# Performance work log

Hardware: AMD Instinct MI355X
Metric: run time of the kernel (lower is better)

## Reference

```python
import jax, jax.numpy as jnp
import numpy as np

CLASSES, SIZE, INPUT_SIZE, CONTEXT_SIZE, BATCH = 8, 512, 512, 512, 64
CMS = 4          # context_map_size -> 2**CMS = 16 contexts per neuron
LR = 0.01
PRED_CLIP = 0.01
WEIGHT_CLIP = 5.0


def _logit(x):
    return jnp.log(x) - jnp.log1p(-x)


def setup_inputs() -> dict:
    key = jax.random.key(0)
    k1, k2, k3, k4, k5 = jax.random.split(key, 5)
    logits = jax.random.normal(k1, (CLASSES, INPUT_SIZE, BATCH), jnp.float32)
    context = jax.random.normal(k2, (BATCH, CONTEXT_SIZE), jnp.float32)
    target = jax.random.uniform(k3, (CLASSES, BATCH), jnp.float32)
    cmaps = jax.random.normal(k4, (CLASSES, SIZE, CMS, CONTEXT_SIZE), jnp.float32)
    cmaps = cmaps / jnp.linalg.norm(cmaps, axis=-1, keepdims=True)
    cbias = jax.random.normal(k5, (CLASSES, SIZE, CMS, 1), jnp.float32)
    weights = jnp.full((CLASSES, SIZE, 2 ** CMS, INPUT_SIZE), 1.0 / INPUT_SIZE, jnp.float32)
    return {"logits": logits, "context": context, "target": target,
            "context_maps": cmaps, "context_bias": cbias, "weights": weights}


def reference(logits, context, target, context_maps, context_bias, weights):
    # --- context hashing ---
    # distances: [classes, size, cms, batch]
    distances = jnp.einsum('cskd,bd->cskb', context_maps, context)
    bits = (distances > context_bias).astype(jnp.int32)
    conv = (2 ** jnp.arange(CMS, dtype=jnp.int32))[:, None]          # [cms, 1]
    idx = jnp.sum(bits * conv, axis=-2)                              # [classes, size, batch]
    # --- gather per-context weights ---
    c = jnp.arange(CLASSES)[:, None, None]
    s = jnp.arange(SIZE)[None, :, None]
    sel = weights[c, s, idx, :]                                      # [classes, size, batch, input]
    # --- per-sample dot product (== diagonal of the original batch x batch matmul) ---
    lo = _logit(jnp.float32(PRED_CLIP))
    hi = _logit(jnp.float32(1.0 - PRED_CLIP))
    out = jnp.clip(jnp.einsum('csbi,cib->csb', sel, logits), lo, hi)  # [classes, size, batch]
    # --- online weight update (clamped) scattered back ---
    sig = jax.nn.sigmoid(out)
    diff = sig - target[:, None, :]                                  # [classes, size, batch]
    # lr * diff[c,s,b] * logits[c,i,b]  -> update [c,s,b,i]
    upd = LR * diff[:, :, :, None] * jnp.transpose(logits, (0, 2, 1))[:, None, :, :]
    new_sel = jnp.clip(sel - upd, -WEIGHT_CLIP, WEIGHT_CLIP)
    new_weights = weights.at[c, s, idx, :].set(new_sel)
    return out, new_weights
```

## Files before the change

kernel.cpp:

```cpp
#include <hip/hip_runtime.h>
#include <math.h>

#define CLASSES 8
#define SIZE 512
#define ISZ 512
#define CSZ 512
#define BATCH 64
#define CMS 4
#define NBUCKET 16
#define LR 0.01f
#define WCLIP 5.0f
#define WSTRIDE 516

typedef float nt_f4 __attribute__((ext_vector_type(4)));

__global__ __launch_bounds__(256) void pack_pre(
    const float* __restrict__ logits,
    const float* __restrict__ context,
    float* __restrict__ Lt,
    float* __restrict__ Lpk,
    float* __restrict__ ctxT4)
{
    __shared__ float t[64][65];
    const int bid  = blockIdx.x;
    const int lane = threadIdx.x & 63;
    const int w    = threadIdx.x >> 6;
    if (bid < 64) {
        const int r0 = bid << 6;
        #pragma unroll
        for (int rep = 0; rep < 16; ++rep) {
            int rr = w * 16 + rep;
            t[rr][lane] = logits[(size_t)(r0 + rr) * 64 + lane];
        }
        __syncthreads();
        const int ci = r0 + lane;
        #pragma unroll
        for (int rep = 0; rep < 16; ++rep) {
            int b = w * 16 + rep;
            float v = t[lane][b];
            Lt[(size_t)b * 4096 + ci] = v;
            Lpk[(size_t)(ci >> 2) * 256 + 4 * b + (ci & 3)] = v;
        }
    } else {
        const int c0 = (bid - 64) << 6;
        #pragma unroll
        for (int rep = 0; rep < 16; ++rep) {
            int rr = w * 16 + rep;
            t[rr][lane] = context[(size_t)rr * 512 + c0 + lane];
        }
        __syncthreads();
        #pragma unroll
        for (int rep = 0; rep < 16; ++rep) {
            int dd = c0 + w * 16 + rep;
            ctxT4[(size_t)(dd >> 2) * 256 + 4 * lane + (dd & 3)] = t[lane][w * 16 + rep];
        }
    }
}

__global__ __launch_bounds__(256, 8) void dist_kernel(
    const float* __restrict__ cmaps,
    const float* __restrict__ cbias,
    const float* __restrict__ ctxT4,
    unsigned char* __restrict__ idxOut)
{
    __shared__ int bits[CMS * BATCH];

    const int tid  = threadIdx.x;
    const int cs   = blockIdx.x;
    const int lane = tid & 63;
    const int wv   = tid >> 6;
    const int k    = __builtin_amdgcn_readfirstlane(wv);

    const float4* cmg = (const float4*)(cmaps + ((size_t)cs * CMS + k) * CSZ);
    {
        const float4* ct4 = (const float4*)ctxT4 + lane;
        float acc = 0.f;
        #pragma unroll 4
        for (int d4 = 0; d4 < 128; ++d4) {
            float4 cm4 = cmg[d4];
            float4 cv  = ct4[(size_t)d4 * 64];
            acc += cm4.x * cv.x + cm4.y * cv.y + cm4.z * cv.z + cm4.w * cv.w;
        }
        float bias = cbias[(size_t)cs * CMS + k];
        bits[k * BATCH + lane] = (acc > bias) ? 1 : 0;
    }
    __syncthreads();

    if (wv == 0) {
        int idx_b = bits[lane] | (bits[BATCH + lane] << 1) |
                    (bits[2 * BATCH + lane] << 2) | (bits[3 * BATCH + lane] << 3);
        idxOut[(size_t)cs * BATCH + lane] = (unsigned char)idx_b;
    }
}

__global__ __launch_bounds__(256, 4) void gln_bc(
    const float* __restrict__ target,
    const float* __restrict__ weights,
    const unsigned char* __restrict__ idxIn,
    const float* __restrict__ Lt,
    const float* __restrict__ Lpk,
    float* __restrict__ out,
    float* __restrict__ outW)
{
    __shared__ float Wl[NBUCKET * WSTRIDE];
    __shared__ float partial[4 * BATCH];
    __shared__ float diff_l[BATCH];

    const int tid  = threadIdx.x;
    const int cs   = blockIdx.x;
    const int c    = cs >> 9;
    const int lane = tid & 63;
    const int wv   = tid >> 6;

    float4 wreg[8];
    const float4* gW = (const float4*)(weights + (size_t)cs * (NBUCKET * ISZ));
    #pragma unroll
    for (int it = 0; it < 8; ++it) wreg[it] = gW[tid + it * 256];

    const int idx_b = idxIn[(size_t)cs * BATCH + lane];

    int blast_r[16];
    #pragma unroll
    for (int j = 0; j < NBUCKET; ++j) {
        unsigned long long m = __ballot(idx_b == j);
        blast_r[j] = m ? (63 - __clzll(m)) : -1;
    }

    const float* LtC = Lt + (size_t)c * ISZ;
    const int col4 = tid & 127;
    const int hi_half = (tid >> 7) & 1;
    float4 lreg[8];
    int    blv[8];
    #pragma unroll
    for (int it = 0; it < 8; ++it) {
        int bl = hi_half ? blast_r[2 * it + 1] : blast_r[2 * it];
        blv[it] = bl;
        int blc = (bl >= 0) ? bl : 0;
        lreg[it] = ((const float4*)(LtC + (size_t)blc * 4096))[col4];
    }

    #pragma unroll
    for (int it = 0; it < 8; ++it) {
        int f = tid + it * 256;
        *(float4*)&Wl[(f >> 7) * WSTRIDE + (f & 127) * 4] = wreg[it];
    }
    __syncthreads();

    {
        const float4* Lp4 = (const float4*)Lpk;
        const int base4 = (c * 128 + wv * 32) * 64 + lane;
        const int wb    = idx_b * WSTRIDE + wv * 128;
        float acc = 0.f;
        #pragma unroll 4
        for (int d4 = 0; d4 < 32; ++d4) {
            float4 w4 = *(const float4*)&Wl[wb + d4 * 4];
            float4 l4 = Lp4[(size_t)base4 + d4 * 64];
            acc += w4.x * l4.x + w4.y * l4.y + w4.z * l4.z + w4.w * l4.w;
        }
        partial[wv * BATCH + lane] = acc;
    }
    __syncthreads();

    if (wv == 0) {
        float s = partial[lane] + partial[BATCH + lane] +
                  partial[2 * BATCH + lane] + partial[3 * BATCH + lane];
        const float hi = 4.595119850134589f;
        float oc = fminf(fmaxf(s, -hi), hi);
        out[(size_t)cs * BATCH + lane] = oc;
        float sig = 1.f / (1.f + expf(-oc));
        diff_l[lane] = LR * (sig - target[c * BATCH + lane]);
    }
    __syncthreads();

    float* gO = outW + (size_t)cs * (NBUCKET * ISZ);
    #pragma unroll
    for (int it = 0; it < 8; ++it) {
        int f = tid + it * 256;
        float4 w4 = wreg[it];
        int bl = blv[it];
        float4 r = w4;
        if (bl >= 0) {
            float coef = diff_l[bl];
            float4 l4  = lreg[it];
            r.x = fminf(fmaxf(w4.x - coef * l4.x, -WCLIP), WCLIP);
            r.y = fminf(fmaxf(w4.y - coef * l4.y, -WCLIP), WCLIP);
            r.z = fminf(fmaxf(w4.z - coef * l4.z, -WCLIP), WCLIP);
            r.w = fminf(fmaxf(w4.w - coef * l4.w, -WCLIP), WCLIP);
        }
        nt_f4 rv; rv.x = r.x; rv.y = r.y; rv.z = r.z; rv.w = r.w;
        __builtin_nontemporal_store(rv, (nt_f4*)gO + f);
    }
}

extern "C" void kernel_launch(void* const* d_in, const int* in_sizes, int n_in,
                              void* d_out, int out_size, void* d_ws, size_t ws_size,
                              hipStream_t stream) {
    const float* logits  = (const float*)d_in[0];
    const float* context = (const float*)d_in[1];
    const float* target  = (const float*)d_in[2];
    const float* cmaps   = (const float*)d_in[3];
    const float* cbias   = (const float*)d_in[4];
    const float* weights = (const float*)d_in[5];

    float* out  = (float*)d_out;
    float* outW = out + (size_t)CLASSES * SIZE * BATCH;

    float* Lt    = (float*)d_ws;
    float* Lpk   = Lt + 262144;
    float* ctxT4 = Lpk + 262144;
    unsigned char* idxb = (unsigned char*)(ctxT4 + 32768);

    pack_pre<<<72, 256, 0, stream>>>(logits, context, Lt, Lpk, ctxT4);
    dist_kernel<<<CLASSES * SIZE, 256, 0, stream>>>(cmaps, cbias, ctxT4, idxb);
    gln_bc<<<CLASSES * SIZE, 256, 0, stream>>>(target, weights, idxb, Lt, Lpk, out, outW);
}
```

Baseline: 131.3 us.

## Halve LDS weight staging and defer logits loads to raise occupancy

The weight tile is now staged through LDS in two half-width passes, which halves shared memory per block. The per-bucket logits row loads are moved from before the dot product to the update loop, which drops the lreg and blv registers. Launch bounds are raised to allow 8 blocks per SM. The nontemporal stores of updated weights become plain float4 stores. The aim is more resident waves to hide the latency of loading and storing the 64 MB weight tensor. The cost is extra barriers and logits loads that now sit on the update path instead of being prefetched.

```diff
diff --git a/kernel.cpp b/kernel.cpp
--- a/kernel.cpp
+++ b/kernel.cpp
@@ -10,9 +10,7 @@
 #define NBUCKET 16
 #define LR 0.01f
 #define WCLIP 5.0f
-#define WSTRIDE 516
-
-typedef float nt_f4 __attribute__((ext_vector_type(4)));
+#define HSTRIDE 260
 
 __global__ __launch_bounds__(256) void pack_pre(
     const float* __restrict__ logits,
@@ -93,7 +91,7 @@
     }
 }
 
-__global__ __launch_bounds__(256, 4) void gln_bc(
+__global__ __launch_bounds__(256, 8) void gln_bc(
     const float* __restrict__ target,
     const float* __restrict__ weights,
     const unsigned char* __restrict__ idxIn,
@@ -102,7 +100,7 @@
     float* __restrict__ out,
     float* __restrict__ outW)
 {
-    __shared__ float Wl[NBUCKET * WSTRIDE];
+    __shared__ float Wl[NBUCKET * HSTRIDE];
     __shared__ float partial[4 * BATCH];
     __shared__ float diff_l[BATCH];
 
@@ -126,39 +124,32 @@
         blast_r[j] = m ? (63 - __clzll(m)) : -1;
     }
 
-    const float* LtC = Lt + (size_t)c * ISZ;
-    const int col4 = tid & 127;
-    const int hi_half = (tid >> 7) & 1;
-    float4 lreg[8];
-    int    blv[8];
-    #pragma unroll
-    for (int it = 0; it < 8; ++it) {
-        int bl = hi_half ? blast_r[2 * it + 1] : blast_r[2 * it];
-        blv[it] = bl;
-        int blc = (bl >= 0) ? bl : 0;
-        lreg[it] = ((const float4*)(LtC + (size_t)blc * 4096))[col4];
-    }
-
-    #pragma unroll
-    for (int it = 0; it < 8; ++it) {
-        int f = tid + it * 256;
-        *(float4*)&Wl[(f >> 7) * WSTRIDE + (f & 127) * 4] = wreg[it];
-    }
-    __syncthreads();
-
-    {
-        const float4* Lp4 = (const float4*)Lpk;
-        const int base4 = (c * 128 + wv * 32) * 64 + lane;
-        const int wb    = idx_b * WSTRIDE + wv * 128;
-        float acc = 0.f;
+    const int col   = tid & 63;
+    const int myrow = tid >> 7;
+    const int stage_par = (tid >> 6) & 1;
+    float acc = 0.f;
+    const float4* Lp4 = (const float4*)Lpk;
+    #pragma unroll
+    for (int h = 0; h < 2; ++h) {
+        if (stage_par == h) {
+            #pragma unroll
+            for (int it = 0; it < 8; ++it) {
+                int row = 2 * it + myrow;
+                *(float4*)&Wl[row * HSTRIDE + col * 4] = wreg[it];
+            }
+        }
+        __syncthreads();
+        const int base4 = (c * 128 + h * 64 + wv * 16) * 64 + lane;
+        const int wb    = idx_b * HSTRIDE + wv * 64;
         #pragma unroll 4
-        for (int d4 = 0; d4 < 32; ++d4) {
+        for (int d4 = 0; d4 < 16; ++d4) {
             float4 w4 = *(const float4*)&Wl[wb + d4 * 4];
             float4 l4 = Lp4[(size_t)base4 + d4 * 64];
             acc += w4.x * l4.x + w4.y * l4.y + w4.z * l4.z + w4.w * l4.w;
         }
-        partial[wv * BATCH + lane] = acc;
-    }
+        __syncthreads();
+    }
+    partial[wv * BATCH + lane] = acc;
     __syncthreads();
 
     if (wv == 0) {
@@ -173,22 +164,24 @@
     __syncthreads();
 
     float* gO = outW + (size_t)cs * (NBUCKET * ISZ);
+    const float* LtC = Lt + (size_t)c * ISZ;
+    const int col4 = tid & 127;
+    const int hi_half = (tid >> 7) & 1;
     #pragma unroll
     for (int it = 0; it < 8; ++it) {
-        int f = tid + it * 256;
+        int f  = tid + it * 256;
+        int bl = hi_half ? blast_r[2 * it + 1] : blast_r[2 * it];
         float4 w4 = wreg[it];
-        int bl = blv[it];
         float4 r = w4;
         if (bl >= 0) {
             float coef = diff_l[bl];
-            float4 l4  = lreg[it];
+            float4 l4  = ((const float4*)(LtC + (size_t)bl * 4096))[col4];
             r.x = fminf(fmaxf(w4.x - coef * l4.x, -WCLIP), WCLIP);
             r.y = fminf(fmaxf(w4.y - coef * l4.y, -WCLIP), WCLIP);
             r.z = fminf(fmaxf(w4.z - coef * l4.z, -WCLIP), WCLIP);
             r.w = fminf(fmaxf(w4.w - coef * l4.w, -WCLIP), WCLIP);
         }
-        nt_f4 rv; rv.x = r.x; rv.y = r.y; rv.z = r.z; rv.w = r.w;
-        __builtin_nontemporal_store(rv, (nt_f4*)gO + f);
+        ((float4*)gO)[f] = r;
     }
 }
 
```

After: 157.5 us. 1.2x slower.
